# Optimization experiments

Hardware: AMD Instinct MI355X
Metric: run time of the kernel (lower is better)

## Reference

```python
import jax, jax.numpy as jnp
import numpy as np

B, T, N, D, FF, E, L, K = 4, 12, 2000, 16, 64, 4, 2, 2
EA, H = 3000, 3
BETA, CW = 0.01, 0.001


def setup_inputs() -> dict:
    key = jax.random.key(0)
    ks = iter(jax.random.split(key, 40))
    nrm = lambda shape, s=0.02: jax.random.normal(next(ks), shape, jnp.float32) * s
    inp = {}
    inp['x'] = jax.random.normal(next(ks), (B, T, N), jnp.float32)
    inp['velo'] = jax.random.uniform(next(ks), (B, T, N), jnp.float32)
    inp['adj_haversine'] = jax.random.uniform(next(ks), (N, N), jnp.float32) + 0.05
    inp['laplacian_diff'] = jax.random.normal(next(ks), (N, N), jnp.float32)
    inp['laplacian_heat'] = jax.random.normal(next(ks), (N, N), jnp.float32)
    inp['start_w'] = nrm((1, D)); inp['start_b'] = jnp.zeros((D,), jnp.float32)
    inp['gate_w'] = nrm((L, D, E))
    inp['exp_w1'] = nrm((L, E, D, FF)); inp['exp_b1'] = jnp.zeros((L, E, FF), jnp.float32)
    inp['exp_w2'] = nrm((L, E, FF, D)); inp['exp_b2'] = jnp.zeros((L, E, D), jnp.float32)
    inp['proj_w'] = nrm((T * D, T)); inp['proj_b'] = jnp.zeros((T,), jnp.float32)
    inp['lt_w'] = nrm((N, EA)); inp['lt_b'] = jnp.zeros((EA,), jnp.float32)
    inp['qkv_w'] = nrm((EA, 3 * EA)); inp['qkv_b'] = jnp.zeros((3 * EA,), jnp.float32)
    inp['attn_out_w'] = nrm((EA, EA)); inp['attn_out_b'] = jnp.zeros((EA,), jnp.float32)
    inp['ll_w'] = nrm((EA, N)); inp['ll_b'] = jnp.zeros((N,), jnp.float32)
    inp['p2_w'] = nrm((T, T)); inp['p2_b'] = jnp.zeros((T,), jnp.float32)
    return inp


def reference(x, velo, adj_haversine, laplacian_diff, laplacian_heat, start_w, start_b,
              gate_w, exp_w1, exp_b1, exp_w2, exp_b2, proj_w, proj_b, lt_w, lt_b,
              qkv_w, qkv_b, attn_out_w, attn_out_b, ll_w, ll_b, p2_w, p2_b):
    # start_fc: [B,T,N,1] -> [B,T,N,D]
    out = x[..., None] @ start_w + start_b
    balance = jnp.float32(0.0)
    cv = lambda v: v.var() / (v.mean() ** 2 + 1e-10)
    for l in range(L):  # AMS mixture-of-experts stack (noisy top-k gating, eval mode)
        feat = out.mean(axis=(1, 2))                      # [B,D]
        logits = feat @ gate_w[l]                          # [B,E]
        topv, topi = jax.lax.top_k(logits, K)
        g = jax.nn.softmax(topv, axis=-1)
        gates = jnp.zeros((B, E), out.dtype).at[jnp.arange(B)[:, None], topi].set(g)
        h = jax.nn.gelu(jnp.einsum('btnd,edf->ebtnf', out, exp_w1[l]) + exp_b1[l][:, None, None, None, :])
        y = jnp.einsum('ebtnf,efd->ebtnd', h, exp_w2[l]) + exp_b2[l][:, None, None, None, :]
        out = out + jnp.einsum('be,ebtnd->btnd', gates, y)  # residual_connection
        imp = gates.sum(0)
        load = (gates > 0).astype(out.dtype).sum(0)
        balance = balance + cv(imp) + cv(load)
    # wavelet layer: 1-level smoothing split along time
    low = lambda z: 0.5 * (z + jnp.roll(z, 1, axis=1))
    low_T = low(x)
    high_V = velo - low(velo)
    # navier-stokes-style graph laplacian from velocities
    v0 = velo[0, 0]                                        # [N]
    G = jnp.maximum(0.0, v0[:, None] / adj_haversine)
    G = jnp.where(jnp.isinf(G), 0.0, G)
    lap_ns = jnp.diag(G.sum(1)) - G
    std = lambda m: (m - m.mean()) / m.std()
    lap_d = std(laplacian_diff); lap_h = std(laplacian_heat)
    lap_ns = jnp.nan_to_num(std(lap_ns))
    # trunk projection: [B,T,N,D] -> [B,T,N]
    outp = (out.transpose(0, 2, 1, 3).reshape(B, N, T * D) @ proj_w + proj_b).transpose(0, 2, 1)
    # laplacian-fused matmuls
    r1 = low_T @ lap_d; r2 = high_V @ lap_ns; r3 = low_T @ lap_h
    rng01 = lambda m: (m - m.min()) / jnp.maximum(m.max() - m.min(), 1e-8)
    lin = lambda m: (rng01(m) @ lt_w + lt_b).transpose(1, 0, 2)   # [T,B,EA]
    r1, r2, r3 = lin(r1), lin(r2), lin(r3)
    hd = EA // H
    wq, wk, wv = jnp.split(qkv_w, 3, axis=1)
    bq, bk, bv = jnp.split(qkv_b, 3)
    def mha(q, k, v):
        qh = (q @ wq + bq).reshape(T, B, H, hd)
        kh = (k @ wk + bk).reshape(T, B, H, hd)
        vh = (v @ wv + bv).reshape(T, B, H, hd)
        sc = jnp.einsum('sbhd,tbhd->bhst', qh, kh) * (1.0 / np.sqrt(hd))
        a = jax.nn.softmax(sc, axis=-1)
        o = jnp.einsum('bhst,tbhd->sbhd', a, vh).reshape(T, B, EA)
        return o @ attn_out_w + attn_out_b
    o1 = mha(r1, r2, r3); o2 = mha(r2, r3, r1); o3 = mha(r3, r1, r2)
    back = lambda o: (o @ ll_w + ll_b).transpose(1, 0, 2)         # [B,T,N]
    out2 = BETA * (back(o1) + back(o2) + back(o3))
    out2 = (out2.reshape(-1, T) @ p2_w + p2_b).reshape(B, N, T).transpose(0, 2, 1)
    out_3 = outp + out2
    # contrastive loss between trunk and laplacian branch
    f1 = outp.transpose(0, 2, 1).reshape(B * N, T)
    f2 = out2.transpose(0, 2, 1).reshape(B * N, T)
    nz = lambda f: f / jnp.maximum(jnp.linalg.norm(f, axis=1, keepdims=True), 1e-12)
    sim = (nz(f1) @ nz(f2).T) / 0.1                               # [8000, 8000]
    closs = -jnp.mean(jnp.diagonal(jax.nn.log_softmax(sim, axis=1)))
    return out_3, balance, CW * closs
```

## Files before the change

kernel.cpp:

```cpp
#include <hip/hip_runtime.h>
#include <math.h>

namespace {
constexpr int B_ = 4, T_ = 12, N_ = 2000, D_ = 16, FF_ = 64, E_ = 4, L_ = 2;
constexpr int EA_ = 3000, H_ = 3, HD_ = EA_ / H_;
constexpr int BT_ = B_ * T_;
constexpr int R3_ = 3 * BT_;
constexpr long long NN_ = (long long)N_ * N_;
constexpr int BTN_ = B_ * T_ * N_;
constexpr float BETA_ = 0.01f, CW_ = 0.001f;
constexpr int RKS_ = 20;
constexpr int RKC_ = 100;
constexpr int KP3 = 3008;
constexpr int KP2 = 2016;

constexpr size_t OFF_OUT4 = 0;
constexpr size_t OFF_LOWT = OFF_OUT4 + (size_t)BTN_ * D_;
constexpr size_t OFF_HVT  = OFF_LOWT + BTN_;
constexpr size_t OFF_ALIN = OFF_HVT + BTN_;
constexpr size_t OFF_RT   = OFF_ALIN + (size_t)N_ * R3_;
constexpr size_t OFF_P    = OFF_RT + (size_t)EA_ * R3_;
constexpr size_t OFF_AOT  = OFF_P + (size_t)R3_ * 3 * EA_;
constexpr size_t OFF_OT   = OFF_AOT + (size_t)EA_ * R3_;
constexpr size_t OFF_O2P  = OFF_OT + (size_t)EA_ * R3_;
constexpr size_t OFF_OUTP = OFF_O2P + BTN_;
constexpr size_t OFF_O2F  = OFF_OUTP + BTN_;
constexpr size_t OFF_LI   = OFF_O2F + BTN_;
constexpr size_t OFF_S    = OFF_LI + 8000;
constexpr size_t OFF_RSL  = OFF_S + 2000;
constexpr size_t OFF_RSH  = OFF_RSL + 48;
constexpr size_t OFF_STP  = OFF_RSH + 48;
constexpr size_t OFF_STAT = OFF_STP + 3072;
constexpr size_t OFF_MMP  = OFF_STAT + 8;
constexpr size_t OFF_AB   = OFF_MMP + 384;
constexpr size_t OFF_CSP  = OFF_AB + 8;
constexpr size_t OFF_CS   = OFF_CSP + 48000;
constexpr size_t OFF_FEAT = OFF_CS + 3000;
constexpr size_t OFF_GATE = OFF_FEAT + 64;
constexpr size_t OFF_BAL  = OFF_GATE + 16;
constexpr size_t OFF_PART = ((OFF_BAL + 1 + 255) & ~(size_t)255);
constexpr size_t PARTCAP  = 13000000;
constexpr size_t OFF_AT_LIN= OFF_PART + PARTCAP;
constexpr size_t OFF_AT_Q  = OFF_AT_LIN + (size_t)R3_ * KP2 / 2;
constexpr size_t OFF_AT_AO = OFF_AT_Q + (size_t)R3_ * KP3 / 2;
constexpr size_t OFF_AT_LL = OFF_AT_AO + (size_t)R3_ * KP3 / 2;
constexpr size_t OFF_G1B   = OFF_AT_LL + (size_t)R3_ * KP3 / 2;
constexpr size_t OFF_G2B   = OFF_G1B + 128000;
}

typedef __attribute__((ext_vector_type(8))) short short8;
typedef __attribute__((ext_vector_type(4))) float f32x4;

__device__ __forceinline__ float waveReduceSum(float v) {
  for (int off = 32; off; off >>= 1) v += __shfl_down(v, off);
  return v;
}

__device__ __forceinline__ unsigned short f2bf(float x) {
  unsigned int u = __float_as_uint(x);
  unsigned int r = (u + 0x7FFFu + ((u >> 16) & 1u)) >> 16;
  return (unsigned short)r;
}

__device__ __forceinline__ size_t aidx(int row, int k) {
  return ((size_t)(k >> 3) * R3_ + row) * 8 + (k & 7);
}

__device__ __forceinline__ void fma16(float* __restrict__ acc,
                                      const float4* __restrict__ a4, float bv) {
#pragma unroll
  for (int r4 = 0; r4 < 4; ++r4) {
    float4 av = a4[r4];
    acc[r4 * 4 + 0] = fmaf(av.x, bv, acc[r4 * 4 + 0]);
    acc[r4 * 4 + 1] = fmaf(av.y, bv, acc[r4 * 4 + 1]);
    acc[r4 * 4 + 2] = fmaf(av.z, bv, acc[r4 * 4 + 2]);
    acc[r4 * 4 + 3] = fmaf(av.w, bv, acc[r4 * 4 + 3]);
  }
}

__global__ void k_init(float* ws) {
  if (threadIdx.x == 0) ws[OFF_BAL] = 0.f;
}

__global__ void k_start(const float* __restrict__ x, const float* __restrict__ sw,
                        const float* __restrict__ sb, float* __restrict__ out4) {
  int i = blockIdx.x * 256 + threadIdx.x;
  if (i >= BTN_ * D_) return;
  int d = i & 15;
  out4[i] = fmaf(x[i >> 4], sw[d], sb[d]);
}

__global__ void k_feat(const float* __restrict__ out4, float* __restrict__ feat) {
  int b = blockIdx.x >> 4, d = blockIdx.x & 15;
  float s = 0.f;
  for (int tn = threadIdx.x; tn < T_ * N_; tn += 256)
    s += out4[((size_t)b * T_ * N_ + tn) * D_ + d];
  __shared__ float red[4];
  s = waveReduceSum(s);
  if ((threadIdx.x & 63) == 0) red[threadIdx.x >> 6] = s;
  __syncthreads();
  if (threadIdx.x == 0)
    feat[blockIdx.x] = (red[0] + red[1] + red[2] + red[3]) * (1.f / (T_ * N_));
}

__global__ void k_gate(const float* __restrict__ feat, const float* __restrict__ gw,
                       float* __restrict__ ws, int l) {
  __shared__ float lg[B_ * E_];
  int tid = threadIdx.x;
  if (tid < B_ * E_) {
    int b = tid >> 2, e = tid & 3;
    float s = 0.f;
    for (int d = 0; d < D_; ++d) s = fmaf(feat[b * D_ + d], gw[(l * D_ + d) * E_ + e], s);
    lg[tid] = s;
  }
  __syncthreads();
  if (tid == 0) {
// ... 70 lines not shown
  int ip = b * T_ * N_ + ((t + T_ - 1) % T_) * N_ + n;
  int row = t * B_ + b;
  lowT[(size_t)n * BT_ + row] = 0.5f * (x[i] + x[ip]);
  hvT[(size_t)n * BT_ + row] = 0.5f * (velo[i] - velo[ip]);
}

__global__ void k_rowsum(const float* __restrict__ lowT, const float* __restrict__ hvT,
                         float* __restrict__ ws) {
  int which = blockIdx.x / BT_;
  int row = blockIdx.x % BT_;
  const float* M = which ? hvT : lowT;
  float s = 0.f;
  for (int n = threadIdx.x; n < N_; n += 256) s += M[(size_t)n * BT_ + row];
  __shared__ float red[4];
  s = waveReduceSum(s);
  if ((threadIdx.x & 63) == 0) red[threadIdx.x >> 6] = s;
  __syncthreads();
  if (threadIdx.x == 0) ws[(which ? OFF_RSH : OFF_RSL) + row] = red[0] + red[1] + red[2] + red[3];
}

__global__ void k_S(const float* __restrict__ adj, const float* __restrict__ v0,
                    float* __restrict__ S) {
  int m = blockIdx.x;
  float vm = v0[m];
  const float* a = adj + (size_t)m * N_;
  float s = 0.f;
  for (int n = threadIdx.x; n < N_; n += 256) s += vm / a[n];
  __shared__ float red[4];
  s = waveReduceSum(s);
  if ((threadIdx.x & 63) == 0) red[threadIdx.x >> 6] = s;
  __syncthreads();
  if (threadIdx.x == 0) S[m] = red[0] + red[1] + red[2] + red[3];
}

__global__ void k_stats2(const float* __restrict__ stp, float* __restrict__ stat) {
  int z = blockIdx.x;
  const float* part = stp + (size_t)z * 1024;
  float s = 0.f, ss = 0.f;
  for (int i = threadIdx.x; i < 160; i += 256) { s += part[i * 2]; ss += part[i * 2 + 1]; }
  __shared__ float r1[4], r2[4];
  for (int off = 32; off; off >>= 1) { s += __shfl_down(s, off); ss += __shfl_down(ss, off); }
  if ((threadIdx.x & 63) == 0) { r1[threadIdx.x >> 6] = s; r2[threadIdx.x >> 6] = ss; }
  __syncthreads();
  if (threadIdx.x == 0) {
    float su = r1[0] + r1[1] + r1[2] + r1[3];
    float sq = r2[0] + r2[1] + r2[2] + r2[3];
    float mu = su * (1.f / (float)NN_);
    float var = sq * (1.f / (float)NN_) - mu * mu;
    stat[2 * z] = mu;
    stat[2 * z + 1] = 1.f / sqrtf(var);
  }
}

__global__ __launch_bounds__(256) void k_rgemm3(
    const float* __restrict__ lowT, const float* __restrict__ hvT,
    const float* __restrict__ lapd, const float* __restrict__ laph,
    const float* __restrict__ adj, const float* __restrict__ v0,
    const float* __restrict__ S, float* __restrict__ part,
    float* __restrict__ stp) {
  int zz = blockIdx.z;
  int z = zz / 3, rg = zz % 3;
  int col = blockIdx.x * 256 + threadIdx.x;
  int m0 = blockIdx.y * RKC_;
  int m1 = min(N_, m0 + RKC_);
  bool doStats = (rg == 0);
  float sAcc = 0.f, ssAcc = 0.f;
  float acc[16];
#pragma unroll
  for (int r = 0; r < 16; ++r) acc[r] = 0.f;
  if (col < N_) {
    const float* Abase = (z == 1 ? hvT : lowT);
    const float* ap = Abase + (size_t)m0 * BT_ + rg * 16;
    if (z != 1) {
      const float* Bm = z ? laph : lapd;
      const float* bp = Bm + (size_t)m0 * N_ + col;
      int len = m1 - m0;
      int ng = len >> 3;
      float bc[8];
      if (ng > 0) {
#pragma unroll
        for (int u = 0; u < 8; ++u) bc[u] = bp[(size_t)u * N_];
      }
      for (int gi = 0; gi < ng; ++gi) {
        float bn[8];
        bool more = (gi + 1 < ng);
        if (more) {
#pragma unroll
          for (int u = 0; u < 8; ++u) bn[u] = bp[(size_t)(8 + u) * N_];
        }
#pragma unroll
        for (int u = 0; u < 8; ++u) {
          fma16(acc, (const float4*)(ap + (size_t)u * BT_), bc[u]);
          if (doStats) { sAcc += bc[u]; ssAcc = fmaf(bc[u], bc[u], ssAcc); }
        }
        ap += (size_t)8 * BT_;
        bp += (size_t)8 * N_;
        if (more) {
#pragma unroll
          for (int u = 0; u < 8; ++u) bc[u] = bn[u];
        }
      }
      for (int m = m0 + (ng << 3); m < m1; ++m) {
        float bv = *bp;
        fma16(acc, (const float4*)ap, bv);
        if (doStats) { sAcc += bv; ssAcc = fmaf(bv, bv, ssAcc); }
        ap += BT_;
// ... 27 lines not shown
        ap += (size_t)8 * BT_;
        jp += (size_t)8 * N_;
        if (more) {
#pragma unroll
          for (int u = 0; u < 8; ++u) jc[u] = jn[u];
        }
      }
      for (; m < m1; ++m) {
        float bv = -(v0[m] / (*jp));
        if (m == col) bv += S[m];
        fma16(acc, (const float4*)ap, bv);
        if (doStats) { sAcc += bv; ssAcc = fmaf(bv, bv, ssAcc); }
        ap += BT_;
        jp += N_;
      }
    }
    float* pp = part + (((size_t)z * RKS_ + blockIdx.y) * BT_ + rg * 16) * N_ + col;
#pragma unroll
    for (int r = 0; r < 16; ++r) pp[(size_t)r * N_] = acc[r];
  }
  if (doStats) {
    __shared__ float r1[4], r2[4];
    float s = sAcc, ss = ssAcc;
    for (int off = 32; off; off >>= 1) { s += __shfl_down(s, off); ss += __shfl_down(ss, off); }
    if ((threadIdx.x & 63) == 0) { r1[threadIdx.x >> 6] = s; r2[threadIdx.x >> 6] = ss; }
    __syncthreads();
    if (threadIdx.x == 0) {
      float* p = stp + (size_t)z * 1024 + ((size_t)blockIdx.y * 8 + blockIdx.x) * 2;
      p[0] = r1[0] + r1[1] + r1[2] + r1[3];
      p[1] = r2[0] + r2[1] + r2[2] + r2[3];
    }
  }
}

__global__ void k_epiR3(const float* __restrict__ part, float* __restrict__ ws,
                        unsigned short* __restrict__ atl) {
  int z = blockIdx.z;
  int n = blockIdx.x * 256 + threadIdx.x;
  int row = blockIdx.y;
  if (n >= KP2) return;
  int arow = z * BT_ + row;
  if (n >= N_) { atl[aidx(arow, n)] = 0; return; }
  const float* base = part + (size_t)z * RKS_ * BT_ * N_;
  float s = 0.f;
  for (int ks = 0; ks < RKS_; ++ks) s += base[((size_t)(ks * BT_ + row)) * N_ + n];
  int statIdx = (z == 0) ? 0 : (z == 1 ? 4 : 2);
  size_t rsOff = (z == 1) ? OFF_RSH : OFF_RSL;
  float mu = ws[OFF_STAT + statIdx], isd = ws[OFF_STAT + statIdx + 1];
  float val = (s - mu * ws[rsOff + row]) * isd;
  ws[OFF_ALIN + (size_t)n * R3_ + arow] = val;
  atl[aidx(arow, n)] = f2bf(val);
}

__global__ __launch_bounds__(256) void k_mfmaW(
    const unsigned short* __restrict__ At, const float* __restrict__ W,
    float* __restrict__ part, int Nc, int Kp, int K, int stepChunk) {
  __shared__ unsigned int lds[2][128][21];
  int tid = threadIdx.x;
  int lane = tid & 63, w = tid >> 6;
  int lr = lane & 15, lo = lane >> 4;
  int colBase = blockIdx.x * 128;
  int stepsTot = Kp / 32;
  int s0 = blockIdx.y * stepChunk;
  int s1 = min(stepsTot, s0 + stepChunk);
  int cg = tid & 31, kr8 = tid >> 5;
  int c0l = 4 * cg;
  bool fullC = (colBase + 128 <= Nc);

  f32x4 acc[18];
#pragma unroll
  for (int mt = 0; mt < 18; ++mt) {
    acc[mt][0] = 0.f; acc[mt][1] = 0.f; acc[mt][2] = 0.f; acc[mt][3] = 0.f;
  }

  auto stage = [&](int s, int buf) {
#pragma unroll
    for (int h = 0; h < 2; ++h) {
      int kp = kr8 + 8 * h;
      int kA = s * 32 + 2 * kp;
      int kB = kA + 1;
      float4 r0 = {0.f, 0.f, 0.f, 0.f}, r1 = {0.f, 0.f, 0.f, 0.f};
      int c0 = colBase + c0l;
      if (fullC) {
        if (kA < K) r0 = *(const float4*)(W + (size_t)kA * Nc + c0);
        if (kB < K) r1 = *(const float4*)(W + (size_t)kB * Nc + c0);
      } else {
        float rr0[4] = {0.f, 0.f, 0.f, 0.f}, rr1[4] = {0.f, 0.f, 0.f, 0.f};
#pragma unroll
        for (int e = 0; e < 4; ++e) {
          if (c0 + e < Nc) {
            if (kA < K) rr0[e] = W[(size_t)kA * Nc + c0 + e];
            if (kB < K) rr1[e] = W[(size_t)kB * Nc + c0 + e];
          }
        }
        r0.x = rr0[0]; r0.y = rr0[1]; r0.z = rr0[2]; r0.w = rr0[3];
        r1.x = rr1[0]; r1.y = rr1[1]; r1.z = rr1[2]; r1.w = rr1[3];
      }
      lds[buf][c0l + 0][kp] = ((unsigned int)f2bf(r1.x) << 16) | f2bf(r0.x);
      lds[buf][c0l + 1][kp] = ((unsigned int)f2bf(r1.y) << 16) | f2bf(r0.y);
      lds[buf][c0l + 2][kp] = ((unsigned int)f2bf(r1.z) << 16) | f2bf(r0.z);
      lds[buf][c0l + 3][kp] = ((unsigned int)f2bf(r1.w) << 16) | f2bf(r0.w);
    }
  };

  if (s0 < s1) stage(s0, 0);
  __syncthreads();

  const unsigned short* ap = At + ((size_t)(s0 * 4 + lo) * R3_ + lr) * 8;
  const size_t apStep = (size_t)4 * R3_ * 8;
  int lcol0 = w * 32 + lr;
  int lcol1 = w * 32 + 16 + lr;
  for (int s = s0; s < s1; ++s) {
    int buf = (s - s0) & 1;
    union { unsigned int u[4]; short8 s8; } b0, b1;
#pragma unroll
    for (int j = 0; j < 4; ++j) {
      b0.u[j] = lds[buf][lcol0][lo * 4 + j];
      b1.u[j] = lds[buf][lcol1][lo * 4 + j];
    }
#pragma unroll
    for (int mt = 0; mt < 9; ++mt) {
      short8 a = *(const short8*)(ap + (size_t)mt * 128);
      acc[mt] = __builtin_amdgcn_mfma_f32_16x16x32_bf16(a, b0.s8, acc[mt], 0, 0, 0);
      acc[9 + mt] = __builtin_amdgcn_mfma_f32_16x16x32_bf16(a, b1.s8, acc[9 + mt], 0, 0, 0);
    }
    if (s + 1 < s1) stage(s + 1, buf ^ 1);
    __syncthreads();
    ap += apStep;
  }

#pragma unroll
  for (int half = 0; half < 2; ++half) {
    int gcol = colBase + w * 32 + half * 16 + lr;
    if (gcol < Nc) {
#pragma unroll
      for (int mt = 0; mt < 9; ++mt) {
        int row = mt * 16 + lo * 4;
        float* pp = part + ((size_t)blockIdx.y * R3_ + row) * Nc + gcol;
        f32x4 a = acc[half * 9 + mt];
        pp[0] = a[0];
        pp[(size_t)Nc] = a[1];
        pp[2 * (size_t)Nc] = a[2];
        pp[3 * (size_t)Nc] = a[3];
      }
    }
  }
}

__global__ void k_minmax(const float* __restrict__ alin, float* __restrict__ mmp) {
  int g = blockIdx.y;
  float mn = 3.4e38f, mx = -3.4e38f;
  for (int i = blockIdx.x * 256 + threadIdx.x; i < N_ * BT_; i += 64 * 256) {
    int n = i / BT_, r = i % BT_;
    float v = alin[(size_t)n * R3_ + g * BT_ + r];
    mn = fminf(mn, v); mx = fmaxf(mx, v);
  }
  __shared__ float rn[4], rx[4];
  for (int off = 32; off; off >>= 1) {
    mn = fminf(mn, __shfl_down(mn, off));
    mx = fmaxf(mx, __shfl_down(mx, off));
  }
  if ((threadIdx.x & 63) == 0) { rn[threadIdx.x >> 6] = mn; rx[threadIdx.x >> 6] = mx; }
  __syncthreads();
  if (threadIdx.x == 0) {
    mn = fminf(fminf(rn[0], rn[1]), fminf(rn[2], rn[3]));
    mx = fmaxf(fmaxf(rx[0], rx[1]), fmaxf(rx[2], rx[3]));
    mmp[(size_t)(g * 64 + blockIdx.x) * 2] = mn;
    mmp[(size_t)(g * 64 + blockIdx.x) * 2 + 1] = mx;
  }
}

__global__ void k_minmax2(float* __restrict__ ws) {
  int g = blockIdx.x;
  int i = threadIdx.x;
  float mn = ws[OFF_MMP + (size_t)(g * 64 + i) * 2];
  float mx = ws[OFF_MMP + (size_t)(g * 64 + i) * 2 + 1];
  for (int off = 32; off; off >>= 1) {
    mn = fminf(mn, __shfl_down(mn, off));
    mx = fmaxf(mx, __shfl_down(mx, off));
  }
  if (i == 0) {
// ... 57 lines not shown
  for (int t = w; t < T_; t += 4) {
    const float* krow = P + ((size_t)(pk[mha] * BT_ + t * B_ + b)) * (3 * EA_) + EA_ + h * HD_;
    float p = 0.f;
    for (int d = lane; d < HD_; d += 64) p = fmaf(qrow[d], krow[d], p);
    p = waveReduceSum(p);
    if (lane == 0) sc[t] = p * 0.031622776601683794f;
  }
  __syncthreads();
  float a[T_];
  float m = sc[0];
#pragma unroll
  for (int t = 1; t < T_; ++t) m = fmaxf(m, sc[t]);
  float sum = 0.f;
#pragma unroll
  for (int t = 0; t < T_; ++t) { a[t] = expf(sc[t] - m); sum += a[t]; }
  float inv = 1.f / sum;
#pragma unroll
  for (int t = 0; t < T_; ++t) a[t] *= inv;
  int orow = mha * BT_ + s_ * B_ + b;
  for (int d = threadIdx.x; d < HD_; d += 256) {
    float o = 0.f;
#pragma unroll
    for (int t = 0; t < T_; ++t)
      o = fmaf(a[t], P[((size_t)(pv[mha] * BT_ + t * B_ + b)) * (3 * EA_) + 2 * EA_ + h * HD_ + d], o);
    atao[aidx(orow, h * HD_ + d)] = f2bf(o);
  }
  if (h == 0 && threadIdx.x < 8) atao[aidx(orow, EA_ + threadIdx.x)] = 0;
}

__global__ void k_epiAO(const float* __restrict__ part, const float* __restrict__ aob,
                        unsigned short* __restrict__ atll, int ksplit) {
  int c = blockIdx.x * 256 + threadIdx.x;
  int row = blockIdx.y;
  if (c >= KP3) return;
  if (c >= EA_) { atll[aidx(row, c)] = 0; return; }
  float s = 0.f;
  for (int ks = 0; ks < ksplit; ++ks) s += part[((size_t)(ks * R3_ + row)) * EA_ + c];
  atll[aidx(row, c)] = f2bf(s + aob[c]);
}

__global__ void k_epiLL(const float* __restrict__ part, const float* __restrict__ llb,
                        float* __restrict__ o2p, int ksplit) {
  int n = blockIdx.x * 256 + threadIdx.x;
  int row = blockIdx.y;
  if (n >= N_) return;
  float s = 0.f;
  for (int g = 0; g < 3; ++g)
    for (int ks = 0; ks < ksplit; ++ks)
      s += part[((size_t)(ks * R3_ + g * BT_ + row)) * N_ + n];
  int t = row / B_, b = row % B_;
  o2p[(size_t)b * (T_ * N_) + t * N_ + n] = BETA_ * (s + 3.f * llb[n]);
}

__global__ void k_proj(const float* __restrict__ out4, const float* __restrict__ pw,
                       const float* __restrict__ pb, float* __restrict__ outp) {
  int i = blockIdx.x * 256 + threadIdx.x;
  if (i >= BTN_) return;
  int b = i / (T_ * N_);
  int t = (i / N_) % T_;
  int n = i % N_;
  float acc = pb[t];
  for (int t2 = 0; t2 < T_; ++t2) {
    const float* o = out4 + ((size_t)(b * T_ + t2) * N_ + n) * D_;
#pragma unroll
    for (int d = 0; d < D_; ++d) acc = fmaf(o[d], pw[(t2 * D_ + d) * T_ + t], acc);
  }
  outp[i] = acc;
}

__global__ void k_p2(const float* __restrict__ o2p, const float* __restrict__ p2w,
                     const float* __restrict__ p2b, float* __restrict__ o2f) {
  int i = blockIdx.x * 256 + threadIdx.x;
  if (i >= BTN_) return;
  int b = i / (T_ * N_);
  int t = (i / N_) % T_;
  int n = i % N_;
  float acc = p2b[t];
  const float* src = o2p + (size_t)b * (T_ * N_) + (size_t)n * T_;
#pragma unroll
  for (int c = 0; c < T_; ++c) acc = fmaf(src[c], p2w[c * T_ + t], acc);
  o2f[i] = acc;
}

__global__ void k_fng(const float* __restrict__ outp, const float* __restrict__ o2f,
                      float* __restrict__ dout, unsigned short* __restrict__ g1b,
                      unsigned short* __restrict__ g2b) {
  int r = blockIdx.x * 256 + threadIdx.x;
  if (r >= B_ * N_) return;
  int b = r / N_, n = r % N_;
  float v1[T_], v2[T_];
  float s1 = 0.f, s2 = 0.f;
#pragma unroll
  for (int t = 0; t < T_; ++t) {
    size_t idx = (size_t)b * T_ * N_ + (size_t)t * N_ + n;
    v1[t] = outp[idx];
    v2[t] = o2f[idx];
    dout[idx] = v1[t] + v2[t];
    s1 = fmaf(v1[t], v1[t], s1);
    s2 = fmaf(v2[t], v2[t], s2);
  }
  float n1 = fmaxf(sqrtf(s1), 1e-12f), n2 = fmaxf(sqrtf(s2), 1e-12f);
  float i1 = 10.f / n1, i2 = 1.f / n2;
  unsigned short q[32], z[32];
#pragma unroll
  for (int t = 0; t < T_; ++t) { q[t] = f2bf(v1[t] * i1); z[t] = f2bf(v2[t] * i2); }
#pragma unroll
  for (int t = T_; t < 32; ++t) { q[t] = 0; z[t] = 0; }
  short8* qd = (short8*)(g1b + (size_t)r * 32);
  short8* zd = (short8*)(g2b + (size_t)r * 32);
#pragma unroll
  for (int c = 0; c < 4; ++c) {
    short8 pv, pz;
#pragma unroll
    for (int e = 0; e < 8; ++e) { pv[e] = (short)q[c * 8 + e]; pz[e] = (short)z[c * 8 + e]; }
    qd[c] = pv;
    zd[c] = pz;
  }
}

__global__ __launch_bounds__(256) void k_lsemf(const unsigned short* __restrict__ g1b,
                                               const unsigned short* __restrict__ g2b,
                                               float* __restrict__ psm,
                                               float* __restrict__ psd) {
  int lane = threadIdx.x & 63, w = threadIdx.x >> 6;
  int lr = lane & 15, lo = lane >> 4;
  int i0 = blockIdx.x * 16;
  int slice = blockIdx.y * 4 + w;
  short8 a = *(const short8*)(g1b + (size_t)(i0 + lr) * 32 + lo * 8);
  float sm[4] = {0.f, 0.f, 0.f, 0.f};
  float sd[4] = {0.f, 0.f, 0.f, 0.f};
  for (int t = slice; t < 500; t += 16) {
    int j0 = t * 16;
    short8 b = *(const short8*)(g2b + (size_t)(j0 + lr) * 32 + lo * 8);
    f32x4 acc = {0.f, 0.f, 0.f, 0.f};
    acc = __builtin_amdgcn_mfma_f32_16x16x32_bf16(a, b, acc, 0, 0, 0);
#pragma unroll
    for (int rg = 0; rg < 4; ++rg) {
      float s = acc[rg];
      sm[rg] += __expf(s);
      if (j0 + lr == i0 + lo * 4 + rg) sd[rg] = s;
    }
  }
#pragma unroll
  for (int off = 1; off < 16; off <<= 1) {
#pragma unroll
    for (int rg = 0; rg < 4; ++rg) {
      sm[rg] += __shfl_xor(sm[rg], off);
      sd[rg] += __shfl_xor(sd[rg], off);
    }
// ... 25 lines not shown
    float sd = psd[r] + psd[8000 + r] + psd[16000 + r] + psd[24000 + r];
    acc += sd - logf(sm);
  }
  __shared__ float red[16];
  acc = waveReduceSum(acc);
  if ((threadIdx.x & 63) == 0) red[threadIdx.x >> 6] = acc;
  __syncthreads();
  if (threadIdx.x == 0) {
    float s = 0.f;
    for (int i = 0; i < 16; ++i) s += red[i];
    float closs = -s * (1.f / (B_ * N_));
    dout[BTN_] = ws[OFF_BAL];
    dout[BTN_ + 1] = CW_ * closs;
  }
}

extern "C" void kernel_launch(void* const* d_in, const int* in_sizes, int n_in,
                              void* d_out, int out_size, void* d_ws, size_t ws_size,
                              hipStream_t stream) {
  const float* x    = (const float*)d_in[0];
  const float* velo = (const float*)d_in[1];
  const float* adj  = (const float*)d_in[2];
  const float* lapd = (const float*)d_in[3];
  const float* laph = (const float*)d_in[4];
  const float* sw   = (const float*)d_in[5];
  const float* sb   = (const float*)d_in[6];
  const float* gw   = (const float*)d_in[7];
  const float* ew1  = (const float*)d_in[8];
  const float* eb1  = (const float*)d_in[9];
  const float* ew2  = (const float*)d_in[10];
  const float* eb2  = (const float*)d_in[11];
  const float* pw   = (const float*)d_in[12];
  const float* pb   = (const float*)d_in[13];
  const float* ltw  = (const float*)d_in[14];
  const float* ltb  = (const float*)d_in[15];
  const float* qkvw = (const float*)d_in[16];
  const float* qkvb = (const float*)d_in[17];
  const float* aow  = (const float*)d_in[18];
  const float* aob  = (const float*)d_in[19];
  const float* llw  = (const float*)d_in[20];
  const float* llb  = (const float*)d_in[21];
  const float* p2w  = (const float*)d_in[22];
  const float* p2b  = (const float*)d_in[23];
  float* ws = (float*)d_ws;
  float* dout = (float*)d_out;
  const float* v0 = velo;
  float* part = ws + OFF_PART;
  unsigned short* atLin = (unsigned short*)(ws + OFF_AT_LIN);
  unsigned short* atQ   = (unsigned short*)(ws + OFF_AT_Q);
  unsigned short* atAO  = (unsigned short*)(ws + OFF_AT_AO);
  unsigned short* atLL  = (unsigned short*)(ws + OFF_AT_LL);
  unsigned short* g1b   = (unsigned short*)(ws + OFF_G1B);
  unsigned short* g2b   = (unsigned short*)(ws + OFF_G2B);
  dim3 b256(256);

  k_init<<<dim3(1), dim3(64), 0, stream>>>(ws);

  k_start<<<dim3((BTN_ * D_ + 255) / 256), b256, 0, stream>>>(x, sw, sb, ws + OFF_OUT4);

  for (int l = 0; l < L_; ++l) {
    k_feat<<<dim3(B_ * D_), b256, 0, stream>>>(ws + OFF_OUT4, ws + OFF_FEAT);
    k_gate<<<dim3(1), dim3(64), 0, stream>>>(ws + OFF_FEAT, gw, ws, l);
    k_expert<<<dim3((T_ * N_ + 255) / 256, B_), b256, 0, stream>>>(ws + OFF_OUT4, ew1, eb1, ew2, eb2, ws, l);
  }

  k_wavelet<<<dim3((BTN_ + 255) / 256), b256, 0, stream>>>(x, velo, ws + OFF_LOWT, ws + OFF_HVT);
  k_rowsum<<<dim3(2 * BT_), b256, 0, stream>>>(ws + OFF_LOWT, ws + OFF_HVT, ws);
  k_S<<<dim3(N_), b256, 0, stream>>>(adj, v0, ws + OFF_S);

  k_rgemm3<<<dim3(8, RKS_, 9), b256, 0, stream>>>(ws + OFF_LOWT, ws + OFF_HVT, lapd, laph,
                                                  adj, v0, ws + OFF_S, part, ws + OFF_STP);
  k_stats2<<<dim3(3), b256, 0, stream>>>(ws + OFF_STP, ws + OFF_STAT);
  k_epiR3<<<dim3(8, 48, 3), b256, 0, stream>>>(part, ws, atLin);

  k_minmax<<<dim3(64, 3), b256, 0, stream>>>(ws + OFF_ALIN, ws + OFF_MMP);
  k_minmax2<<<dim3(3), dim3(64), 0, stream>>>(ws);
  k_colsum<<<dim3(12, 16), b256, 0, stream>>>(ltw, ws + OFF_CSP);
  k_colsum2<<<dim3(12), b256, 0, stream>>>(ws);

  k_mfmaW<<<dim3(24, 16), b256, 0, stream>>>(atLin, ltw, part, EA_, KP2, N_, 4);
  k_epiLin<<<dim3(12, 144), b256, 0, stream>>>(part, ltb, ws, atQ, 16);

  k_mfmaW<<<dim3(71, 10), b256, 0, stream>>>(atQ, qkvw, part, 3 * EA_, KP3, EA_, 10);
  k_epiQkv<<<dim3(36, 144), b256, 0, stream>>>(part, qkvb, ws + OFF_P, 10);

  k_attn<<<dim3(T_ * B_ * H_, 3), b256, 0, stream>>>(ws + OFF_P, atAO);

  k_mfmaW<<<dim3(24, 16), b256, 0, stream>>>(atAO, aow, part, EA_, KP3, EA_, 6);
  k_epiAO<<<dim3(12, 144), b256, 0, stream>>>(part, aob, atLL, 16);

  k_mfmaW<<<dim3(16, 20), b256, 0, stream>>>(atLL, llw, part, N_, KP3, EA_, 5);
  k_epiLL<<<dim3(8, 48), b256, 0, stream>>>(part, llb, ws + OFF_O2P, 20);

  k_proj<<<dim3((BTN_ + 255) / 256), b256, 0, stream>>>(ws + OFF_OUT4, pw, pb, ws + OFF_OUTP);
  k_p2<<<dim3((BTN_ + 255) / 256), b256, 0, stream>>>(ws + OFF_O2P, p2w, p2b, ws + OFF_O2F);

  k_fng<<<dim3((B_ * N_ + 255) / 256), b256, 0, stream>>>(ws + OFF_OUTP, ws + OFF_O2F, dout, g1b, g2b);

  k_lsemf<<<dim3(500, 4), b256, 0, stream>>>(g1b, g2b, part, part + 32000);
  k_lsefin<<<dim3(1), dim3(1024), 0, stream>>>(part, part + 32000, ws, dout);
}
```

Measured before the change: 501.1 us.

## Pre-transpose weights to bf16 K-packed layout and drop LDS staging in MFMA GEMMs

Adds a k_wt kernel that converts each fp32 weight matrix once per call into a bf16 layout packed in groups of 8 along K, matching the MFMA B-operand format. The GEMM kernel then loads B fragments directly from global memory as short8, with no LDS double buffering and no per-step __syncthreads. This removes the in-loop fp32-to-bf16 conversion and the synchronisation. In exchange it runs four extra transpose kernels that read about 60M floats of weights on every call, and B fragments are no longer shared through LDS across waves.

```diff
diff --git a/kernel.cpp b/kernel.cpp
--- a/kernel.cpp
+++ b/kernel.cpp
@@ -46,6 +46,10 @@
 constexpr size_t OFF_AT_LL = OFF_AT_AO + (size_t)R3_ * KP3 / 2;
 constexpr size_t OFF_G1B   = OFF_AT_LL + (size_t)R3_ * KP3 / 2;
 constexpr size_t OFF_G2B   = OFF_G1B + 128000;
+constexpr size_t OFF_WTL   = OFF_G2B + 128000;
+constexpr size_t OFF_WTQ   = OFF_WTL + (size_t)EA_ * KP2 / 2;
+constexpr size_t OFF_WTA   = OFF_WTQ + (size_t)3 * EA_ * KP3 / 2;
+constexpr size_t OFF_WTLL  = OFF_WTA + (size_t)EA_ * KP3 / 2;
 }
 
 typedef __attribute__((ext_vector_type(8))) short short8;
@@ -238,6 +242,29 @@
   }
 }
 
+__global__ void k_wt(const float* __restrict__ W, unsigned short* __restrict__ Wt,
+                     int K, int Nc) {
+  __shared__ float t[32][65];
+  int c0 = blockIdx.x * 64;
+  int k0 = blockIdx.y * 32;
+  int c = threadIdx.x & 63, kk = threadIdx.x >> 6;
+#pragma unroll
+  for (int j = 0; j < 8; ++j) {
+    int k = kk * 8 + j;
+    int gk = k0 + k, gc = c0 + c;
+    float v = 0.f;
+    if (gk < K && gc < Nc) v = W[(size_t)gk * Nc + gc];
+    t[k][c] = v;
+  }
+  __syncthreads();
+  int col = c0 + c;
+  if (col >= Nc) return;
+  short8 v;
+#pragma unroll
+  for (int j = 0; j < 8; ++j) v[j] = (short)f2bf(t[kk * 8 + j][c]);
+  *(short8*)(Wt + ((size_t)(k0 / 8 + kk) * Nc + col) * 8) = v;
+}
+
 __global__ __launch_bounds__(256) void k_rgemm3(
     const float* __restrict__ lowT, const float* __restrict__ hvT,
     const float* __restrict__ lapd, const float* __restrict__ laph,
@@ -371,20 +398,20 @@
   atl[aidx(arow, n)] = f2bf(val);
 }
 
-__global__ __launch_bounds__(256) void k_mfmaW(
-    const unsigned short* __restrict__ At, const float* __restrict__ W,
-    float* __restrict__ part, int Nc, int Kp, int K, int stepChunk) {
-  __shared__ unsigned int lds[2][128][21];
+__global__ __launch_bounds__(256) void k_mfmaB(
+    const unsigned short* __restrict__ At, const unsigned short* __restrict__ Bt,
+    float* __restrict__ part, int Nc, int Kp, int stepChunk) {
   int tid = threadIdx.x;
   int lane = tid & 63, w = tid >> 6;
   int lr = lane & 15, lo = lane >> 4;
   int colBase = blockIdx.x * 128;
+  int col0 = colBase + w * 32 + lr;
+  int col1 = col0 + 16;
+  int c0 = min(col0, Nc - 1);
+  int c1 = min(col1, Nc - 1);
   int stepsTot = Kp / 32;
   int s0 = blockIdx.y * stepChunk;
   int s1 = min(stepsTot, s0 + stepChunk);
-  int cg = tid & 31, kr8 = tid >> 5;
-  int c0l = 4 * cg;
-  bool fullC = (colBase + 128 <= Nc);
 
   f32x4 acc[18];
 #pragma unroll
@@ -392,60 +419,23 @@
     acc[mt][0] = 0.f; acc[mt][1] = 0.f; acc[mt][2] = 0.f; acc[mt][3] = 0.f;
   }
 
-  auto stage = [&](int s, int buf) {
-#pragma unroll
-    for (int h = 0; h < 2; ++h) {
-      int kp = kr8 + 8 * h;
-      int kA = s * 32 + 2 * kp;
-      int kB = kA + 1;
-      float4 r0 = {0.f, 0.f, 0.f, 0.f}, r1 = {0.f, 0.f, 0.f, 0.f};
-      int c0 = colBase + c0l;
-      if (fullC) {
-        if (kA < K) r0 = *(const float4*)(W + (size_t)kA * Nc + c0);
-        if (kB < K) r1 = *(const float4*)(W + (size_t)kB * Nc + c0);
-      } else {
-        float rr0[4] = {0.f, 0.f, 0.f, 0.f}, rr1[4] = {0.f, 0.f, 0.f, 0.f};
-#pragma unroll
-        for (int e = 0; e < 4; ++e) {
-          if (c0 + e < Nc) {
-            if (kA < K) rr0[e] = W[(size_t)kA * Nc + c0 + e];
-            if (kB < K) rr1[e] = W[(size_t)kB * Nc + c0 + e];
-          }
-        }
-        r0.x = rr0[0]; r0.y = rr0[1]; r0.z = rr0[2]; r0.w = rr0[3];
-        r1.x = rr1[0]; r1.y = rr1[1]; r1.z = rr1[2]; r1.w = rr1[3];
-      }
-      lds[buf][c0l + 0][kp] = ((unsigned int)f2bf(r1.x) << 16) | f2bf(r0.x);
-      lds[buf][c0l + 1][kp] = ((unsigned int)f2bf(r1.y) << 16) | f2bf(r0.y);
-      lds[buf][c0l + 2][kp] = ((unsigned int)f2bf(r1.z) << 16) | f2bf(r0.z);
-      lds[buf][c0l + 3][kp] = ((unsigned int)f2bf(r1.w) << 16) | f2bf(r0.w);
-    }
-  };
-
-  if (s0 < s1) stage(s0, 0);
-  __syncthreads();
-
   const unsigned short* ap = At + ((size_t)(s0 * 4 + lo) * R3_ + lr) * 8;
+  const unsigned short* bp0 = Bt + ((size_t)(s0 * 4 + lo) * Nc + c0) * 8;
+  const unsigned short* bp1 = Bt + ((size_t)(s0 * 4 + lo) * Nc + c1) * 8;
   const size_t apStep = (size_t)4 * R3_ * 8;
-  int lcol0 = w * 32 + lr;
-  int lcol1 = w * 32 + 16 + lr;
+  const size_t bStep = (size_t)4 * Nc * 8;
   for (int s = s0; s < s1; ++s) {
-    int buf = (s - s0) & 1;
-    union { unsigned int u[4]; short8 s8; } b0, b1;
-#pragma unroll
-    for (int j = 0; j < 4; ++j) {
-      b0.u[j] = lds[buf][lcol0][lo * 4 + j];
-      b1.u[j] = lds[buf][lcol1][lo * 4 + j];
-    }
+    short8 b0 = *(const short8*)bp0;
+    short8 b1 = *(const short8*)bp1;
 #pragma unroll
     for (int mt = 0; mt < 9; ++mt) {
       short8 a = *(const short8*)(ap + (size_t)mt * 128);
-      acc[mt] = __builtin_amdgcn_mfma_f32_16x16x32_bf16(a, b0.s8, acc[mt], 0, 0, 0);
-      acc[9 + mt] = __builtin_amdgcn_mfma_f32_16x16x32_bf16(a, b1.s8, acc[9 + mt], 0, 0, 0);
+      acc[mt] = __builtin_amdgcn_mfma_f32_16x16x32_bf16(a, b0, acc[mt], 0, 0, 0);
+      acc[9 + mt] = __builtin_amdgcn_mfma_f32_16x16x32_bf16(a, b1, acc[9 + mt], 0, 0, 0);
     }
-    if (s + 1 < s1) stage(s + 1, buf ^ 1);
-    __syncthreads();
     ap += apStep;
+    bp0 += bStep;
+    bp1 += bStep;
   }
 
 #pragma unroll
@@ -783,9 +773,18 @@
   unsigned short* atLL  = (unsigned short*)(ws + OFF_AT_LL);
   unsigned short* g1b   = (unsigned short*)(ws + OFF_G1B);
   unsigned short* g2b   = (unsigned short*)(ws + OFF_G2B);
+  unsigned short* wtL   = (unsigned short*)(ws + OFF_WTL);
+  unsigned short* wtQ   = (unsigned short*)(ws + OFF_WTQ);
+  unsigned short* wtA   = (unsigned short*)(ws + OFF_WTA);
+  unsigned short* wtLL  = (unsigned short*)(ws + OFF_WTLL);
   dim3 b256(256);
 
   k_init<<<dim3(1), dim3(64), 0, stream>>>(ws);
+
+  k_wt<<<dim3(47, 63), b256, 0, stream>>>(ltw, wtL, N_, EA_);
+  k_wt<<<dim3(141, 94), b256, 0, stream>>>(qkvw, wtQ, EA_, 3 * EA_);
+  k_wt<<<dim3(47, 94), b256, 0, stream>>>(aow, wtA, EA_, EA_);
+  k_wt<<<dim3(32, 94), b256, 0, stream>>>(llw, wtLL, EA_, N_);
 
   k_start<<<dim3((BTN_ * D_ + 255) / 256), b256, 0, stream>>>(x, sw, sb, ws + OFF_OUT4);
 
@@ -809,18 +808,18 @@
   k_colsum<<<dim3(12, 16), b256, 0, stream>>>(ltw, ws + OFF_CSP);
   k_colsum2<<<dim3(12), b256, 0, stream>>>(ws);
 
-  k_mfmaW<<<dim3(24, 16), b256, 0, stream>>>(atLin, ltw, part, EA_, KP2, N_, 4);
+  k_mfmaB<<<dim3(24, 16), b256, 0, stream>>>(atLin, wtL, part, EA_, KP2, 4);
   k_epiLin<<<dim3(12, 144), b256, 0, stream>>>(part, ltb, ws, atQ, 16);
 
-  k_mfmaW<<<dim3(71, 10), b256, 0, stream>>>(atQ, qkvw, part, 3 * EA_, KP3, EA_, 10);
+  k_mfmaB<<<dim3(71, 10), b256, 0, stream>>>(atQ, wtQ, part, 3 * EA_, KP3, 10);
   k_epiQkv<<<dim3(36, 144), b256, 0, stream>>>(part, qkvb, ws + OFF_P, 10);
 
   k_attn<<<dim3(T_ * B_ * H_, 3), b256, 0, stream>>>(ws + OFF_P, atAO);
 
-  k_mfmaW<<<dim3(24, 16), b256, 0, stream>>>(atAO, aow, part, EA_, KP3, EA_, 6);
+  k_mfmaB<<<dim3(24, 16), b256, 0, stream>>>(atAO, wtA, part, EA_, KP3, 6);
   k_epiAO<<<dim3(12, 144), b256, 0, stream>>>(part, aob, atLL, 16);
 
-  k_mfmaW<<<dim3(16, 20), b256, 0, stream>>>(atLL, llw, part, N_, KP3, EA_, 5);
+  k_mfmaB<<<dim3(16, 20), b256, 0, stream>>>(atLL, wtLL, part, N_, KP3, 5);
   k_epiLL<<<dim3(8, 48), b256, 0, stream>>>(part, llb, ws + OFF_O2P, 20);
 
   k_proj<<<dim3((BTN_ + 255) / 256), b256, 0, stream>>>(ws + OFF_OUT4, pw, pb, ws + OFF_OUTP);
```

Result: slower. 553.7 us (+10.5%).

## Prefetch weight tiles two steps ahead in registers in MFMA GEMM

Applied to the files above, without the earlier changes.

Restructures the k_mfmaW main loop so the global loads of fp32 weight tiles for step s+2 go into registers while MFMAs for step s run. The bf16 conversion and LDS write are deferred until just before the barrier, which is meant to hide global memory latency behind compute. It also cuts the split-K count for the QKV GEMM from 10 to 8 chunks of 12 steps each, which means fewer partial sums to reduce in the epilogue. The cost is more live registers and fewer blocks for the QKV GEMM.

```diff
diff --git a/kernel.cpp b/kernel.cpp
--- a/kernel.cpp
+++ b/kernel.cpp
@@ -62,6 +62,10 @@
   return (unsigned short)r;
 }
 
+__device__ __forceinline__ unsigned int pk2(float hi, float lo) {
+  return ((unsigned int)f2bf(hi) << 16) | f2bf(lo);
+}
+
 __device__ __forceinline__ size_t aidx(int row, int k) {
   return ((size_t)(k >> 3) * R3_ + row) * 8 + (k & 7);
 }
@@ -392,14 +396,14 @@
     acc[mt][0] = 0.f; acc[mt][1] = 0.f; acc[mt][2] = 0.f; acc[mt][3] = 0.f;
   }
 
-  auto stage = [&](int s, int buf) {
+  auto loadStep = [&](int s, float4& r00, float4& r10, float4& r01, float4& r11) {
+    int c0 = colBase + c0l;
 #pragma unroll
     for (int h = 0; h < 2; ++h) {
       int kp = kr8 + 8 * h;
       int kA = s * 32 + 2 * kp;
       int kB = kA + 1;
       float4 r0 = {0.f, 0.f, 0.f, 0.f}, r1 = {0.f, 0.f, 0.f, 0.f};
-      int c0 = colBase + c0l;
       if (fullC) {
         if (kA < K) r0 = *(const float4*)(W + (size_t)kA * Nc + c0);
         if (kB < K) r1 = *(const float4*)(W + (size_t)kB * Nc + c0);
@@ -415,22 +419,25 @@
         r0.x = rr0[0]; r0.y = rr0[1]; r0.z = rr0[2]; r0.w = rr0[3];
         r1.x = rr1[0]; r1.y = rr1[1]; r1.z = rr1[2]; r1.w = rr1[3];
       }
-      lds[buf][c0l + 0][kp] = ((unsigned int)f2bf(r1.x) << 16) | f2bf(r0.x);
-      lds[buf][c0l + 1][kp] = ((unsigned int)f2bf(r1.y) << 16) | f2bf(r0.y);
-      lds[buf][c0l + 2][kp] = ((unsigned int)f2bf(r1.z) << 16) | f2bf(r0.z);
-      lds[buf][c0l + 3][kp] = ((unsigned int)f2bf(r1.w) << 16) | f2bf(r0.w);
+      if (h == 0) { r00 = r0; r10 = r1; } else { r01 = r0; r11 = r1; }
     }
   };
 
-  if (s0 < s1) stage(s0, 0);
-  __syncthreads();
-
-  const unsigned short* ap = At + ((size_t)(s0 * 4 + lo) * R3_ + lr) * 8;
-  const size_t apStep = (size_t)4 * R3_ * 8;
+  auto writeLds = [&](int buf, const float4& r00, const float4& r10,
+                      const float4& r01, const float4& r11) {
+    lds[buf][c0l + 0][kr8] = pk2(r10.x, r00.x);
+    lds[buf][c0l + 1][kr8] = pk2(r10.y, r00.y);
+    lds[buf][c0l + 2][kr8] = pk2(r10.z, r00.z);
+    lds[buf][c0l + 3][kr8] = pk2(r10.w, r00.w);
+    lds[buf][c0l + 0][kr8 + 8] = pk2(r11.x, r01.x);
+    lds[buf][c0l + 1][kr8 + 8] = pk2(r11.y, r01.y);
+    lds[buf][c0l + 2][kr8 + 8] = pk2(r11.z, r01.z);
+    lds[buf][c0l + 3][kr8 + 8] = pk2(r11.w, r01.w);
+  };
+
   int lcol0 = w * 32 + lr;
   int lcol1 = w * 32 + 16 + lr;
-  for (int s = s0; s < s1; ++s) {
-    int buf = (s - s0) & 1;
+  auto mfmaStep = [&](int buf, const unsigned short* ap) {
     union { unsigned int u[4]; short8 s8; } b0, b1;
 #pragma unroll
     for (int j = 0; j < 4; ++j) {
@@ -443,9 +450,27 @@
       acc[mt] = __builtin_amdgcn_mfma_f32_16x16x32_bf16(a, b0.s8, acc[mt], 0, 0, 0);
       acc[9 + mt] = __builtin_amdgcn_mfma_f32_16x16x32_bf16(a, b1.s8, acc[9 + mt], 0, 0, 0);
     }
-    if (s + 1 < s1) stage(s + 1, buf ^ 1);
+  };
+
+  float4 A00, A10, A01, A11, B00, B10, B01, B11;
+  if (s0 < s1) loadStep(s0, A00, A10, A01, A11);
+  if (s0 + 1 < s1) loadStep(s0 + 1, B00, B10, B01, B11);
+
+  const unsigned short* ap = At + ((size_t)(s0 * 4 + lo) * R3_ + lr) * 8;
+  const size_t apStep = (size_t)4 * R3_ * 8;
+  for (int s = s0; s < s1; s += 2) {
+    writeLds(0, A00, A10, A01, A11);
     __syncthreads();
+    if (s + 2 < s1) loadStep(s + 2, A00, A10, A01, A11);
+    mfmaStep(0, ap);
     ap += apStep;
+    if (s + 1 < s1) {
+      writeLds(1, B00, B10, B01, B11);
+      __syncthreads();
+      if (s + 3 < s1) loadStep(s + 3, B00, B10, B01, B11);
+      mfmaStep(1, ap);
+      ap += apStep;
+    }
   }
 
 #pragma unroll
@@ -812,8 +837,8 @@
   k_mfmaW<<<dim3(24, 16), b256, 0, stream>>>(atLin, ltw, part, EA_, KP2, N_, 4);
   k_epiLin<<<dim3(12, 144), b256, 0, stream>>>(part, ltb, ws, atQ, 16);
 
-  k_mfmaW<<<dim3(71, 10), b256, 0, stream>>>(atQ, qkvw, part, 3 * EA_, KP3, EA_, 10);
-  k_epiQkv<<<dim3(36, 144), b256, 0, stream>>>(part, qkvb, ws + OFF_P, 10);
+  k_mfmaW<<<dim3(71, 8), b256, 0, stream>>>(atQ, qkvw, part, 3 * EA_, KP3, EA_, 12);
+  k_epiQkv<<<dim3(36, 144), b256, 0, stream>>>(part, qkvb, ws + OFF_P, 8);
 
   k_attn<<<dim3(T_ * B_ * H_, 3), b256, 0, stream>>>(ws + OFF_P, atAO);
 
```

Measured after the change: 502.2 us. About the same (+0.2%).

## Halve MFMA column tile for weight GEMMs and fuse proj, p2 and normalize kernels

Applied to the files above, without the earlier changes.

Adds a 64-column variant of the bf16 MFMA weight GEMM and uses it for the lt, attention-out and ll projections, doubling the grid so more CUs are busy. The original 128-column kernel is kept as k_mfmaWq for the large QKV GEMM. The separate proj, p2 and norm/pack kernels are merged into one per-row kernel that computes all T outputs in registers, which removes the intermediate outp/o2f round trips and two launches. The tradeoff is fewer MFMAs per staged B tile and a small 64-thread block for the fused kernel.

```diff
diff --git a/kernel.cpp b/kernel.cpp
--- a/kernel.cpp
+++ b/kernel.cpp
@@ -374,6 +374,88 @@
 __global__ __launch_bounds__(256) void k_mfmaW(
     const unsigned short* __restrict__ At, const float* __restrict__ W,
     float* __restrict__ part, int Nc, int Kp, int K, int stepChunk) {
+  __shared__ unsigned int lds[2][64][21];
+  int tid = threadIdx.x;
+  int lane = tid & 63, w = tid >> 6;
+  int lr = lane & 15, lo = lane >> 4;
+  int colBase = blockIdx.x * 64;
+  int gcol = colBase + w * 16 + lr;
+  int stepsTot = Kp / 32;
+  int s0 = blockIdx.y * stepChunk;
+  int s1 = min(stepsTot, s0 + stepChunk);
+  int cg = tid & 15, kr2 = tid >> 4;
+  int c0l = 4 * cg;
+  bool fullC = (colBase + 64 <= Nc);
+
+  f32x4 acc[9];
+#pragma unroll
+  for (int mt = 0; mt < 9; ++mt) {
+    acc[mt][0] = 0.f; acc[mt][1] = 0.f; acc[mt][2] = 0.f; acc[mt][3] = 0.f;
+  }
+
+  auto stage = [&](int s, int buf) {
+    int kA = s * 32 + 2 * kr2;
+    int kB = kA + 1;
+    float4 r0 = {0.f, 0.f, 0.f, 0.f}, r1 = {0.f, 0.f, 0.f, 0.f};
+    int c0 = colBase + c0l;
+    if (fullC) {
+      if (kA < K) r0 = *(const float4*)(W + (size_t)kA * Nc + c0);
+      if (kB < K) r1 = *(const float4*)(W + (size_t)kB * Nc + c0);
+    } else {
+      float rr0[4] = {0.f, 0.f, 0.f, 0.f}, rr1[4] = {0.f, 0.f, 0.f, 0.f};
+#pragma unroll
+      for (int e = 0; e < 4; ++e) {
+        if (c0 + e < Nc) {
+          if (kA < K) rr0[e] = W[(size_t)kA * Nc + c0 + e];
+          if (kB < K) rr1[e] = W[(size_t)kB * Nc + c0 + e];
+        }
+      }
+      r0.x = rr0[0]; r0.y = rr0[1]; r0.z = rr0[2]; r0.w = rr0[3];
+      r1.x = rr1[0]; r1.y = rr1[1]; r1.z = rr1[2]; r1.w = rr1[3];
+    }
+    lds[buf][c0l + 0][kr2] = ((unsigned int)f2bf(r1.x) << 16) | f2bf(r0.x);
+    lds[buf][c0l + 1][kr2] = ((unsigned int)f2bf(r1.y) << 16) | f2bf(r0.y);
+    lds[buf][c0l + 2][kr2] = ((unsigned int)f2bf(r1.z) << 16) | f2bf(r0.z);
+    lds[buf][c0l + 3][kr2] = ((unsigned int)f2bf(r1.w) << 16) | f2bf(r0.w);
+  };
+
+  if (s0 < s1) stage(s0, 0);
+  __syncthreads();
+
+  const unsigned short* ap = At + ((size_t)(s0 * 4 + lo) * R3_ + lr) * 8;
+  int lcol = w * 16 + lr;
+  for (int s = s0; s < s1; ++s) {
+    int buf = (s - s0) & 1;
+    union { unsigned int u[4]; short8 s8; } bu;
+#pragma unroll
+    for (int j = 0; j < 4; ++j) bu.u[j] = lds[buf][lcol][lo * 4 + j];
+    short8 b = bu.s8;
+#pragma unroll
+    for (int mt = 0; mt < 9; ++mt) {
+      short8 a = *(const short8*)(ap + (size_t)mt * 128);
+      acc[mt] = __builtin_amdgcn_mfma_f32_16x16x32_bf16(a, b, acc[mt], 0, 0, 0);
+    }
+    if (s + 1 < s1) stage(s + 1, buf ^ 1);
+    __syncthreads();
+    ap += (size_t)4 * R3_ * 8;
+  }
+
+  if (gcol < Nc) {
+#pragma unroll
+    for (int mt = 0; mt < 9; ++mt) {
+      int row = mt * 16 + lo * 4;
+      float* pp = part + ((size_t)blockIdx.y * R3_ + row) * Nc + gcol;
+      pp[0] = acc[mt][0];
+      pp[(size_t)Nc] = acc[mt][1];
+      pp[2 * (size_t)Nc] = acc[mt][2];
+      pp[3 * (size_t)Nc] = acc[mt][3];
+    }
+  }
+}
+
+__global__ __launch_bounds__(256) void k_mfmaWq(
+    const unsigned short* __restrict__ At, const float* __restrict__ W,
+    float* __restrict__ part, int Nc, int Kp, int K, int stepChunk) {
   __shared__ unsigned int lds[2][128][21];
   int tid = threadIdx.x;
   int lane = tid & 63, w = tid >> 6;
@@ -609,49 +691,42 @@
   o2p[(size_t)b * (T_ * N_) + t * N_ + n] = BETA_ * (s + 3.f * llb[n]);
 }
 
-__global__ void k_proj(const float* __restrict__ out4, const float* __restrict__ pw,
-                       const float* __restrict__ pb, float* __restrict__ outp) {
-  int i = blockIdx.x * 256 + threadIdx.x;
-  if (i >= BTN_) return;
-  int b = i / (T_ * N_);
-  int t = (i / N_) % T_;
-  int n = i % N_;
-  float acc = pb[t];
+__global__ void k_ppf(const float* __restrict__ out4, const float* __restrict__ pw,
+                      const float* __restrict__ pb, const float* __restrict__ o2p,
+                      const float* __restrict__ p2w, const float* __restrict__ p2b,
+                      float* __restrict__ dout, unsigned short* __restrict__ g1b,
+                      unsigned short* __restrict__ g2b) {
+  int r = blockIdx.x * 64 + threadIdx.x;
+  if (r >= B_ * N_) return;
+  int b = r / N_, n = r % N_;
+  float v1[T_];
+#pragma unroll
+  for (int t = 0; t < T_; ++t) v1[t] = pb[t];
   for (int t2 = 0; t2 < T_; ++t2) {
     const float* o = out4 + ((size_t)(b * T_ + t2) * N_ + n) * D_;
 #pragma unroll
-    for (int d = 0; d < D_; ++d) acc = fmaf(o[d], pw[(t2 * D_ + d) * T_ + t], acc);
-  }
-  outp[i] = acc;
-}
-
-__global__ void k_p2(const float* __restrict__ o2p, const float* __restrict__ p2w,
-                     const float* __restrict__ p2b, float* __restrict__ o2f) {
-  int i = blockIdx.x * 256 + threadIdx.x;
-  if (i >= BTN_) return;
-  int b = i / (T_ * N_);
-  int t = (i / N_) % T_;
-  int n = i % N_;
-  float acc = p2b[t];
+    for (int d = 0; d < D_; ++d) {
+      float od = o[d];
+      const float* pr = pw + (t2 * D_ + d) * T_;
+#pragma unroll
+      for (int t = 0; t < T_; ++t) v1[t] = fmaf(od, pr[t], v1[t]);
+    }
+  }
   const float* src = o2p + (size_t)b * (T_ * N_) + (size_t)n * T_;
-#pragma unroll
-  for (int c = 0; c < T_; ++c) acc = fmaf(src[c], p2w[c * T_ + t], acc);
-  o2f[i] = acc;
-}
-
-__global__ void k_fng(const float* __restrict__ outp, const float* __restrict__ o2f,
-                      float* __restrict__ dout, unsigned short* __restrict__ g1b,
-                      unsigned short* __restrict__ g2b) {
-  int r = blockIdx.x * 256 + threadIdx.x;
-  if (r >= B_ * N_) return;
-  int b = r / N_, n = r % N_;
-  float v1[T_], v2[T_];
+  float v2[T_];
+#pragma unroll
+  for (int t = 0; t < T_; ++t) v2[t] = p2b[t];
+#pragma unroll
+  for (int c = 0; c < T_; ++c) {
+    float sc = src[c];
+    const float* pr = p2w + c * T_;
+#pragma unroll
+    for (int t = 0; t < T_; ++t) v2[t] = fmaf(sc, pr[t], v2[t]);
+  }
   float s1 = 0.f, s2 = 0.f;
 #pragma unroll
   for (int t = 0; t < T_; ++t) {
     size_t idx = (size_t)b * T_ * N_ + (size_t)t * N_ + n;
-    v1[t] = outp[idx];
-    v2[t] = o2f[idx];
     dout[idx] = v1[t] + v2[t];
     s1 = fmaf(v1[t], v1[t], s1);
     s2 = fmaf(v2[t], v2[t], s2);
@@ -809,24 +884,23 @@
   k_colsum<<<dim3(12, 16), b256, 0, stream>>>(ltw, ws + OFF_CSP);
   k_colsum2<<<dim3(12), b256, 0, stream>>>(ws);
 
-  k_mfmaW<<<dim3(24, 16), b256, 0, stream>>>(atLin, ltw, part, EA_, KP2, N_, 4);
+  k_mfmaW<<<dim3(47, 16), b256, 0, stream>>>(atLin, ltw, part, EA_, KP2, N_, 4);
   k_epiLin<<<dim3(12, 144), b256, 0, stream>>>(part, ltb, ws, atQ, 16);
 
-  k_mfmaW<<<dim3(71, 10), b256, 0, stream>>>(atQ, qkvw, part, 3 * EA_, KP3, EA_, 10);
+  k_mfmaWq<<<dim3(71, 10), b256, 0, stream>>>(atQ, qkvw, part, 3 * EA_, KP3, EA_, 10);
   k_epiQkv<<<dim3(36, 144), b256, 0, stream>>>(part, qkvb, ws + OFF_P, 10);
 
   k_attn<<<dim3(T_ * B_ * H_, 3), b256, 0, stream>>>(ws + OFF_P, atAO);
 
-  k_mfmaW<<<dim3(24, 16), b256, 0, stream>>>(atAO, aow, part, EA_, KP3, EA_, 6);
+  k_mfmaW<<<dim3(47, 16), b256, 0, stream>>>(atAO, aow, part, EA_, KP3, EA_, 6);
   k_epiAO<<<dim3(12, 144), b256, 0, stream>>>(part, aob, atLL, 16);
 
-  k_mfmaW<<<dim3(16, 20), b256, 0, stream>>>(atLL, llw, part, N_, KP3, EA_, 5);
+  k_mfmaW<<<dim3(32, 20), b256, 0, stream>>>(atLL, llw, part, N_, KP3, EA_, 5);
   k_epiLL<<<dim3(8, 48), b256, 0, stream>>>(part, llb, ws + OFF_O2P, 20);
 
-  k_proj<<<dim3((BTN_ + 255) / 256), b256, 0, stream>>>(ws + OFF_OUT4, pw, pb, ws + OFF_OUTP);
-  k_p2<<<dim3((BTN_ + 255) / 256), b256, 0, stream>>>(ws + OFF_O2P, p2w, p2b, ws + OFF_O2F);
-
-  k_fng<<<dim3((B_ * N_ + 255) / 256), b256, 0, stream>>>(ws + OFF_OUTP, ws + OFF_O2F, dout, g1b, g2b);
+  k_ppf<<<dim3((B_ * N_ + 63) / 64), dim3(64), 0, stream>>>(ws + OFF_OUT4, pw, pb,
+                                                            ws + OFF_O2P, p2w, p2b,
+                                                            dout, g1b, g2b);
 
   k_lsemf<<<dim3(500, 4), b256, 0, stream>>>(g1b, g2b, part, part + 32000);
   k_lsefin<<<dim3(1), dim3(1024), 0, stream>>>(part, part + 32000, ws, dout);
```

Result: faster. 483.3 us (median of 2 runs) (-3.6%).
